# Optimization experiments

Measured on AMD Instinct MI355X. Metric: run time of the kernel, lower is better.

The kernel has to match this reference:

```python
import jax, jax.numpy as jnp
import numpy as np

D_MODEL, D_STATE, EXPAND = 768, 16, 2
D_INNER = D_MODEL * EXPAND
B, L = 2, 2048


def setup_inputs() -> dict:
    key = jax.random.key(0)
    ks = jax.random.split(key, 10)
    s = 0.02  # init scale for projection weights
    return {
        "x": jax.random.normal(ks[0], (B, L, D_MODEL), jnp.float32),
        "in_w": jax.random.normal(ks[1], (D_MODEL, 2 * D_INNER), jnp.float32) * s,
        "conv_w": jax.random.normal(ks[2], (D_INNER, 1, 3), jnp.float32) * 0.1,
        "conv_b": jnp.zeros((D_INNER,), jnp.float32),
        "xproj_w": jax.random.normal(ks[3], (D_INNER, 2 * D_STATE), jnp.float32) * s,
        "dt_w": jax.random.normal(ks[4], (D_INNER, D_INNER), jnp.float32) * s,
        "dt_b": jnp.zeros((D_INNER,), jnp.float32),
        "A_log": jax.random.normal(ks[5], (D_INNER, D_STATE), jnp.float32) * 0.01,
        "D": jnp.ones((D_INNER,), jnp.float32),
        "out_w": jax.random.normal(ks[6], (D_INNER, D_MODEL), jnp.float32) * s,
    }


def reference(x, in_w, conv_w, conv_b, xproj_w, dt_w, dt_b, A_log, D, out_w):
    d_inner = conv_w.shape[0]
    d_state = A_log.shape[1]

    xz = x @ in_w                                   # [B,L,2*d_inner]
    x_c, z = jnp.split(xz, 2, axis=-1)

    # depthwise conv1d, kernel 3, padding 1
    xc = jnp.transpose(x_c, (0, 2, 1))              # [B,d_inner,L]
    xc = jax.lax.conv_general_dilated(
        xc, conv_w, window_strides=(1,), padding=[(1, 1)],
        feature_group_count=d_inner,
        dimension_numbers=("NCH", "OIH", "NCH"))
    xc = xc + conv_b[None, :, None]
    xc = jax.nn.silu(jnp.transpose(xc, (0, 2, 1)))  # [B,L,d_inner]

    Bs, Cs = jnp.split(xc @ xproj_w, 2, axis=-1)    # each [B,L,d_state]
    delta = jax.nn.softplus(xc @ dt_w + dt_b)       # [B,L,d_inner]
    A = -jnp.exp(A_log.astype(jnp.float32))         # [d_inner,d_state]

    deltaA = jnp.exp(jnp.einsum("bld,dn->bldn", delta, A))      # [B,L,d_inner,d_state]
    deltaBx = jnp.einsum("bld,bln->bldn", delta * xc, Bs)        # [B,L,d_inner,d_state]

    def step(h, inp):
        dA_t, dBx_t, c_t = inp                      # [B,d,n],[B,d,n],[B,n]
        h = dA_t * h + dBx_t
        y_t = jnp.einsum("bdn,bn->bd", h, c_t)
        return h, y_t

    h0 = jnp.zeros((x.shape[0], d_inner, d_state), xc.dtype)
    xs = (jnp.moveaxis(deltaA, 1, 0), jnp.moveaxis(deltaBx, 1, 0), jnp.moveaxis(Cs, 1, 0))
    _, ys = jax.lax.scan(step, h0, xs)              # ys: [L,B,d_inner]
    y = jnp.moveaxis(ys, 0, 1) + D * xc             # skip connection

    y = y * jax.nn.silu(z)
    return y @ out_w                                # [B,L,d_model]
```

## Files before the change

### kernel.cpp

```cpp
#include <hip/hip_runtime.h>
#include <cmath>

#define DMODEL 768
#define DINNER 1536
#define NSTATE 16
#define SEQL   2048
#define NCHUNK 32
#define CHLEN  64

#define DT_F32  0
#define DT_BF16 1
#define DT_ZERO 2

typedef __bf16 bf16x8 __attribute__((ext_vector_type(8)));
typedef float  f32x4  __attribute__((ext_vector_type(4)));

typedef __attribute__((address_space(3))) unsigned short lds_us;
typedef const __attribute__((address_space(1))) unsigned short glob_us;

__device__ __forceinline__ void async_cp16(glob_us* g, lds_us* l) {
    __builtin_amdgcn_global_load_lds((const __attribute__((address_space(1))) void*)g,
                                     (__attribute__((address_space(3))) void*)l, 16, 0, 0);
}

__device__ __forceinline__ float bf2f(unsigned short h) {
    union { unsigned u; float f; } v; v.u = ((unsigned)h) << 16; return v.f;
}
__device__ __forceinline__ float bflo(unsigned p) {
    union { unsigned u; float f; } v; v.u = p << 16; return v.f;
}
__device__ __forceinline__ float bfhi(unsigned p) {
    union { unsigned u; float f; } v; v.u = p & 0xFFFF0000u; return v.f;
}
__device__ __forceinline__ unsigned short f2bf(float f) {
    union { float f; unsigned u; } v; v.f = f;
    unsigned r = (v.u + 0x7FFFu + ((v.u >> 16) & 1u)) >> 16;
    return (unsigned short)r;
}
__device__ __forceinline__ float quad_reduce(float y) {
    int yi = __float_as_int(y);
    y += __int_as_float(__builtin_amdgcn_mov_dpp(yi, 0xB1, 0xF, 0xF, true));
    yi = __float_as_int(y);
    y += __int_as_float(__builtin_amdgcn_mov_dpp(yi, 0x4E, 0xF, 0xF, true));
    return y;
}
__device__ int detect_dtype(const void* p) {
    const unsigned* u = (const unsigned*)p;
    int nzlo = 0, band = 0, anynz = 0;
    for (int i = 0; i < 64; ++i) {
        unsigned w = u[i];
        anynz |= (w != 0);
        unsigned lo = w & 0xFFFFu;
        if (lo) {
            ++nzlo;
            unsigned e8 = (lo >> 7) & 0xFF;
            if (e8 >= 0x60 && e8 <= 0x8E) ++band;
        }
    }
    if (nzlo >= 8) return (band * 2 > nzlo) ? DT_BF16 : DT_F32;
    return anynz ? DT_F32 : DT_ZERO;
}
__device__ __forceinline__ float LD(const void* p, size_t i, int dt) {
    if (dt == DT_BF16) return bf2f(((const unsigned short*)p)[i]);
    if (dt == DT_F32)  return ((const float*)p)[i];
    return 0.f;
}

__global__ __launch_bounds__(256) void prep_kernel(
    const void* __restrict__ x, const void* __restrict__ in_w,
    const void* __restrict__ cw, const void* __restrict__ cb,
    const void* __restrict__ xp, const void* __restrict__ dt_w,
    const void* __restrict__ db, const void* __restrict__ Al,
    const void* __restrict__ Dv, const void* __restrict__ out_w,
    unsigned short* __restrict__ xb, unsigned short* __restrict__ inT,
    unsigned short* __restrict__ dtT, unsigned short* __restrict__ outT,
    float* __restrict__ pf)
{
    __shared__ unsigned short tile[64][68];
    __shared__ int dts[6];
    const int blk = blockIdx.x;
    const int t   = threadIdx.x;

    if (blk < 324) {
        if (t == 0) {
            dts[0] = detect_dtype(cw); dts[1] = detect_dtype(cb);
            dts[2] = detect_dtype(db); dts[3] = detect_dtype(Al);
            dts[4] = detect_dtype(Dv); dts[5] = detect_dtype(xp);
        }
        __syncthreads();
        int g = blk * 256 + t;
        if (g >= 82944) return;
        const void* src; int local; int which;
        if      (g <  4608) { src = cw; local = g;         which = 0; }
        else if (g <  6144) { src = cb; local = g - 4608;  which = 1; }
        else if (g <  7680) { src = db; local = g - 6144;  which = 2; }
        else if (g < 32256) { src = Al; local = g - 7680;  which = 3; }
        else if (g < 33792) { src = Dv; local = g - 32256; which = 4; }
        else                { src = xp; local = g - 33792; which = 5; }
        float v = LD(src, local, dts[which]);
        int out = g;
        if (which == 3) v = -__expf(v) * 1.44269504f;
        if (which == 0) out = (local % 3) * DINNER + local / 3;
        pf[out] = v;
    } else if (blk < 1860) {
        if (t == 0) dts[0] = detect_dtype(x);
        __syncthreads();
        const int dt = dts[0];
        size_t i = ((size_t)(blk - 324) * 256 + t) * 8;
        ushort4 o0, o1;
        if (dt == DT_F32) {
            float4 a = *(const float4*)((const float*)x + i);
            float4 b = *(const float4*)((const float*)x + i + 4);
            o0.x = f2bf(a.x); o0.y = f2bf(a.y); o0.z = f2bf(a.z); o0.w = f2bf(a.w);
            o1.x = f2bf(b.x); o1.y = f2bf(b.y); o1.z = f2bf(b.z); o1.w = f2bf(b.w);
        } else if (dt == DT_BF16) {
            o0 = *(const ushort4*)((const unsigned short*)x + i);
            o1 = *(const ushort4*)((const unsigned short*)x + i + 4);
        } else {
            o0 = (ushort4){0,0,0,0}; o1 = (ushort4){0,0,0,0};
        }
        *(ushort4*)&xb[i] = o0;
        *(ushort4*)&xb[i + 4] = o1;
    } else {
        const void* src; unsigned short* dst; int R, C, tx_n, idx;
        if (blk < 2436)      { src = in_w;  dst = inT;  R = 768;  C = 3072; tx_n = 48; idx = blk - 1860; }
        else if (blk < 3012) { src = dt_w;  dst = dtT;  R = 1536; C = 1536; tx_n = 24; idx = blk - 2436; }
        else                 { src = out_w; dst = outT; R = 1536; C = 768;  tx_n = 12; idx = blk - 3012; }
        if (t == 0) dts[0] = detect_dtype(src);
        __syncthreads();
        const int dt = dts[0];
        const int tx = t & 15, ty = t >> 4;
        const int bx = (idx % tx_n) * 64, by = (idx / tx_n) * 64;
        #pragma unroll
        for (int i = 0; i < 4; ++i) {
            int rl = ty + i * 16;
            size_t soff = (size_t)(by + rl) * C + bx + tx * 4;
            ushort4 hv;
            if (dt == DT_F32) {
                float4 v = *(const float4*)((const float*)src + soff);
                hv.x = f2bf(v.x); hv.y = f2bf(v.y); hv.z = f2bf(v.z); hv.w = f2bf(v.w);
            } else if (dt == DT_BF16) {
                hv = *(const ushort4*)((const unsigned short*)src + soff);
            } else {
                hv = (ushort4){0,0,0,0};
            }
            *(ushort4*)&tile[rl][tx * 4] = hv;
        }
        __syncthreads();
        #pragma unroll
        for (int i = 0; i < 4; ++i) {
            int cl = ty + i * 16;
            int m0 = tx * 4;
            ushort4 o;
            o.x = tile[m0 + 0][cl]; o.y = tile[m0 + 1][cl];
            o.z = tile[m0 + 2][cl]; o.w = tile[m0 + 3][cl];
            *(ushort4*)&dst[(size_t)(bx + cl) * R + by + m0] = o;
        }
    }
}

template<int EPI>
__global__ __launch_bounds__(256) void gemm_kernel(
    const unsigned short* __restrict__ A, const unsigned short* __restrict__ Bt,
    void* __restrict__ C0, void* __restrict__ C1, const float* __restrict__ biasf,
    int M, int N, int K)
{
    __shared__ __align__(16) unsigned short As[2][2][128 * 32];
    __shared__ __align__(16) unsigned short Bs[2][2][64 * 32];
    const int t    = threadIdx.x;
    const int m0   = blockIdx.x * 128;
    const int n0   = blockIdx.y * 64;
    const int w    = t >> 6;
    const int lane = t & 63;
    const int wm   = (w >> 1) * 64, wn = (w & 1) * 32;
    const int lm   = lane & 15, quad = lane >> 4;
    const int srow = lane >> 2;
    const int sg   = lane & 3;

    f32x4 acc[4][2] = {};

    auto stage = [&](int k0, int q) {
        #pragma unroll
        for (int ph = 0; ph < 2; ++ph) {
            #pragma unroll
            for (int h = 0; h < 2; ++h) {
                int row = w * 32 + h * 16 + srow;
                int kg  = (sg - (row >> 1)) & 3;
                async_cp16((glob_us*)&A[(size_t)(m0 + row) * K + k0 + ph * 32 + kg * 8],
                           (lds_us*)&As[q][ph][(w * 32 + h * 16) * 32]);
            }
            int brow = w * 16 + srow;
            int bkg  = (sg - (brow >> 1)) & 3;
            async_cp16((glob_us*)&Bt[(size_t)(n0 + brow) * K + k0 + ph * 32 + bkg * 8],
                       (lds_us*)&Bs[q][ph][(w * 16) * 32]);
        }
    };

    stage(0, 0);

    int p = 0;
    for (int k0 = 0; k0 < K; k0 += 64) {
        __syncthreads();
        if (k0 + 64 < K) stage(k0 + 64, p ^ 1);
        #pragma unroll
        for (int ph = 0; ph < 2; ++ph) {
            bf16x8 af[4], bfr[2];
            #pragma unroll
            for (int i = 0; i < 4; ++i) {
                int row = wm + i * 16 + lm;
                int g   = (quad + (row >> 1)) & 3;
                af[i] = *(const bf16x8*)&As[p][ph][row * 32 + g * 8];
            }
            #pragma unroll
            for (int j = 0; j < 2; ++j) {
                int row = wn + j * 16 + lm;
                int g   = (quad + (row >> 1)) & 3;
                bfr[j] = *(const bf16x8*)&Bs[p][ph][row * 32 + g * 8];
            }
            #pragma unroll
            for (int i = 0; i < 4; ++i)
                #pragma unroll
                for (int j = 0; j < 2; ++j)
                    acc[i][j] = __builtin_amdgcn_mfma_f32_16x16x32_bf16(af[i], bfr[j], acc[i][j], 0, 0, 0);
        }
        p ^= 1;
    }

    const int half = N >> 1;
    #pragma unroll
    for (int i = 0; i < 4; ++i) {
        #pragma unroll
        for (int j = 0; j < 2; ++j) {
            int col = n0 + wn + j * 16 + lm;
            #pragma unroll
            for (int r = 0; r < 4; ++r) {
                int row = m0 + wm + i * 16 + quad * 4 + r;
                float v = acc[i][j][r];
                if (EPI == 1) {
                    v += biasf[col];
                    float sp = (v > 20.f) ? v : log1pf(__expf(v));
                    ((unsigned short*)C0)[(size_t)row * N + col] = f2bf(sp);
                } else if (EPI == 2) {
                    ((float*)C0)[(size_t)row * N + col] = v;
                } else {
                    if (col < half) {
                        ((unsigned short*)C0)[(size_t)row * half + col] = f2bf(v);
                    } else {
                        float s = v / (1.f + __expf(-v));
                        ((unsigned short*)C1)[(size_t)row * half + col - half] = f2bf(s);
                    }
                }
            }
        }
    }
}

__global__ __launch_bounds__(256) void conv_silu_kernel(
    const unsigned short* __restrict__ xcpre, const float* __restrict__ cwf,
    const float* __restrict__ cbf, unsigned short* __restrict__ xcb)
{
    const float* cw0 = cwf;
    const float* cw1 = cwf + DINNER;
    const float* cw2 = cwf + 2 * DINNER;
    size_t idx = ((size_t)blockIdx.x * 256 + threadIdx.x) * 8;
    int d8  = (int)(idx % DINNER);
    int row = (int)(idx / DINNER);
    int l   = row % SEQL;
    size_t base = (size_t)row * DINNER + d8;
    uint4 zero = {0, 0, 0, 0};
    uint4 xm = (l > 0)        ? *(const uint4*)&xcpre[base - DINNER] : zero;
    uint4 x0 = *(const uint4*)&xcpre[base];
    uint4 xp = (l < SEQL - 1) ? *(const uint4*)&xcpre[base + DINNER] : zero;
    float4 c0a = *(const float4*)&cw0[d8], c0b = *(const float4*)&cw0[d8 + 4];
    float4 c1a = *(const float4*)&cw1[d8], c1b = *(const float4*)&cw1[d8 + 4];
    float4 c2a = *(const float4*)&cw2[d8], c2b = *(const float4*)&cw2[d8 + 4];
    float4 cba = *(const float4*)&cbf[d8], cbb = *(const float4*)&cbf[d8 + 4];
    const unsigned* mw = (const unsigned*)&xm;
    const unsigned* zw = (const unsigned*)&x0;
    const unsigned* pw = (const unsigned*)&xp;
    const float* C0 = (const float*)&c0a;
    float w0[8] = {c0a.x, c0a.y, c0a.z, c0a.w, c0b.x, c0b.y, c0b.z, c0b.w};
    float w1[8] = {c1a.x, c1a.y, c1a.z, c1a.w, c1b.x, c1b.y, c1b.z, c1b.w};
    float w2[8] = {c2a.x, c2a.y, c2a.z, c2a.w, c2b.x, c2b.y, c2b.z, c2b.w};
    float bb[8] = {cba.x, cba.y, cba.z, cba.w, cbb.x, cbb.y, cbb.z, cbb.w};
    (void)C0;
    unsigned short out[8];
    #pragma unroll
    for (int k = 0; k < 8; ++k) {
        unsigned wm_ = mw[k >> 1], wz = zw[k >> 1], wp = pw[k >> 1];
        float a = (k & 1) ? bfhi(wm_) : bflo(wm_);
        float c = (k & 1) ? bfhi(wz)  : bflo(wz);
        float e = (k & 1) ? bfhi(wp)  : bflo(wp);
        float acc = bb[k] + a * w0[k] + c * w1[k] + e * w2[k];
        float s = acc / (1.f + __expf(-acc));
        out[k] = f2bf(s);
    }
    *(uint4*)&xcb[base] = *(uint4*)out;
}

__global__ __launch_bounds__(128) void xproj_kernel(
    const unsigned short* __restrict__ xcb, const float* __restrict__ wf,
    float* __restrict__ BC)
{
    __shared__ float red[4][32][4];
    const int t = threadIdx.x;
    const int s = t & 31, part = t >> 5;
    const int row0 = blockIdx.x * 4;
    float acc[4] = {0.f, 0.f, 0.f, 0.f};
    for (int k = part * 384; k < (part + 1) * 384; ++k) {
        float wv = wf[k * 32 + s];
        #pragma unroll
        for (int r = 0; r < 4; ++r)
            acc[r] += bf2f(xcb[(size_t)(row0 + r) * DINNER + k]) * wv;
    }
    #pragma unroll
    for (int r = 0; r < 4; ++r) red[part][s][r] = acc[r];
    __syncthreads();
    if (t < 32) {
        #pragma unroll
        for (int r = 0; r < 4; ++r)
            BC[(size_t)(row0 + r) * 32 + t] =
                red[0][t][r] + red[1][t][r] + red[2][t][r] + red[3][t][r];
    }
}

struct GrpA { unsigned dv2[4], xv2[4]; f32x4 Bv[4]; };
struct GrpC { unsigned dv2[4], xv2[4]; f32x4 Bv[4], Cv[4]; };

__device__ __forceinline__ void ldA(GrpA& gp, const unsigned short* pd,
    const unsigned short* px, const float* pbc, int l) {
    #pragma unroll
    for (int j = 0; j < 4; ++j) {
        size_t o = (size_t)(l + j) * DINNER;
        gp.dv2[j] = *(const unsigned*)&pd[o];
        gp.xv2[j] = *(const unsigned*)&px[o];
        gp.Bv[j]  = *(const f32x4*)&pbc[(size_t)(l + j) * 32];
    }
}
__device__ __forceinline__ void ldC(GrpC& gp, const unsigned short* pd,
    const unsigned short* px, const float* pbc, int l) {
    #pragma unroll
    for (int j = 0; j < 4; ++j) {
        size_t o = (size_t)(l + j) * DINNER;
        gp.dv2[j] = *(const unsigned*)&pd[o];
        gp.xv2[j] = *(const unsigned*)&px[o];
        gp.Bv[j]  = *(const f32x4*)&pbc[(size_t)(l + j) * 32];
        gp.Cv[j]  = *(const f32x4*)&pbc[(size_t)(l + j) * 32 + 16];
    }
}
__device__ __forceinline__ void stepA(const GrpA& gp, const f32x4 A2a,
    const f32x4 A2b, f32x4& h0, f32x4& h1, float& sdv0, float& sdv1) {
    #pragma unroll
    for (int j = 0; j < 4; ++j) {
        float dv0 = bflo(gp.dv2[j]), dv1 = bfhi(gp.dv2[j]);
        float xv0 = bflo(gp.xv2[j]), xv1 = bfhi(gp.xv2[j]);
        sdv0 += dv0; sdv1 += dv1;
        f32x4 Bv = gp.Bv[j];
        f32x4 e0, e1;
        e0[0] = __builtin_amdgcn_exp2f(dv0 * A2a[0]);
        e0[1] = __builtin_amdgcn_exp2f(dv0 * A2a[1]);
        e0[2] = __builtin_amdgcn_exp2f(dv0 * A2a[2]);
        e0[3] = __builtin_amdgcn_exp2f(dv0 * A2a[3]);
        e1[0] = __builtin_amdgcn_exp2f(dv1 * A2b[0]);
        e1[1] = __builtin_amdgcn_exp2f(dv1 * A2b[1]);
        e1[2] = __builtin_amdgcn_exp2f(dv1 * A2b[2]);
        e1[3] = __builtin_amdgcn_exp2f(dv1 * A2b[3]);
        h0 = e0 * h0 + (dv0 * xv0) * Bv;
        h1 = e1 * h1 + (dv1 * xv1) * Bv;
    }
}

__global__ __launch_bounds__(256) void scan_phase_a(
    const unsigned short* __restrict__ dlt, const unsigned short* __restrict__ xcb,
    const float* __restrict__ BC, const float* __restrict__ A_log_f,
    unsigned short* __restrict__ P, float* __restrict__ S)
{
    const int t   = threadIdx.x;
    const int q   = t & 3;
    const int dpl = t >> 2;
    const int bid = blockIdx.x;
    const int dg  = bid % 12;
    const int cc  = (bid / 12) % NCHUNK;
    const int b   = bid / (12 * NCHUNK);
    const int d   = (dg * 64 + dpl) * 2;
    f32x4 A2a = *(const f32x4*)&A_log_f[d * 16 + q * 4];
    f32x4 A2b = *(const f32x4*)&A_log_f[(d + 1) * 16 + q * 4];
    f32x4 h0 = (f32x4){0.f, 0.f, 0.f, 0.f};
    f32x4 h1 = (f32x4){0.f, 0.f, 0.f, 0.f};
    float sdv0 = 0.f, sdv1 = 0.f;
    const int row0 = b * SEQL + cc * CHLEN;
    const unsigned short* pd = dlt + (size_t)row0 * DINNER + d;
    const unsigned short* px = xcb + (size_t)row0 * DINNER + d;
    const float* pbc = BC + (size_t)row0 * 32 + q * 4;

    GrpA ga, gb;
    ldA(ga, pd, px, pbc, 0);
    for (int l0 = 0; l0 < CHLEN; l0 += 8) {
        ldA(gb, pd, px, pbc, l0 + 4);
        stepA(ga, A2a, A2b, h0, h1, sdv0, sdv1);
        if (l0 + 8 < CHLEN) ldA(ga, pd, px, pbc, l0 + 8);
        stepA(gb, A2a, A2b, h0, h1, sdv0, sdv1);
    }

    size_t idx = (((size_t)(b * NCHUNK + cc)) * DINNER + d) * 16 + q * 4;
    *(f32x4*)&S[idx] = h0;
    *(f32x4*)&S[idx + 16] = h1;
    ushort4 p0, p1;
    p0.x = f2bf(__builtin_amdgcn_exp2f(sdv0 * A2a[0]));
    p0.y = f2bf(__builtin_amdgcn_exp2f(sdv0 * A2a[1]));
    p0.z = f2bf(__builtin_amdgcn_exp2f(sdv0 * A2a[2]));
    p0.w = f2bf(__builtin_amdgcn_exp2f(sdv0 * A2a[3]));
    p1.x = f2bf(__builtin_amdgcn_exp2f(sdv1 * A2b[0]));
    p1.y = f2bf(__builtin_amdgcn_exp2f(sdv1 * A2b[1]));
    p1.z = f2bf(__builtin_amdgcn_exp2f(sdv1 * A2b[2]));
    p1.w = f2bf(__builtin_amdgcn_exp2f(sdv1 * A2b[3]));
    *(ushort4*)&P[idx] = p0;
    *(ushort4*)&P[idx + 16] = p1;
}

__global__ __launch_bounds__(256) void scan_combine(
    const unsigned short* __restrict__ P, float* __restrict__ S)
{
    int t = blockIdx.x * 256 + threadIdx.x;
    int b = t / (DINNER * NSTATE);
    int dn = t % (DINNER * NSTATE);
    const size_t stride = (size_t)(DINNER * NSTATE);
    size_t idx = (size_t)b * NCHUNK * stride + dn;
    float Pv = bf2f(P[idx]);
    float Sv = S[idx];
    float H = 0.f;
    for (int c = 0; c < NCHUNK; ++c) {
        float Pn = 0.f, Sn = 0.f;
        if (c + 1 < NCHUNK) {
            Pn = bf2f(P[idx + stride]);
            Sn = S[idx + stride];
        }
        S[idx] = H;
        H = Pv * H + Sv;
        Pv = Pn; Sv = Sn;
        idx += stride;
    }
}

__global__ __launch_bounds__(256) void scan_phase_c(
    const unsigned short* __restrict__ dlt, const unsigned short* __restrict__ xcb,
    const float* __restrict__ BC, const unsigned short* __restrict__ zg,
    const float* __restrict__ A_log_f, const float* __restrict__ D_f,
    const float* __restrict__ Hin, unsigned short* __restrict__ yg)
{
    const int t   = threadIdx.x;
    const int q   = t & 3;
    const int dpl = t >> 2;
    const int bid = blockIdx.x;
    const int dg  = bid % 12;
    const int cc  = (bid / 12) % NCHUNK;
    const int b   = bid / (12 * NCHUNK);
    const int d   = (dg * 64 + dpl) * 2;
    f32x4 A2a = *(const f32x4*)&A_log_f[d * 16 + q * 4];
    f32x4 A2b = *(const f32x4*)&A_log_f[(d + 1) * 16 + q * 4];
    size_t hidx = (((size_t)(b * NCHUNK + cc)) * DINNER + d) * 16 + q * 4;
    f32x4 h0 = *(const f32x4*)&Hin[hidx];
    f32x4 h1 = *(const f32x4*)&Hin[hidx + 16];
    const float Dd0 = D_f[d], Dd1 = D_f[d + 1];
    const int row0 = b * SEQL + cc * CHLEN;
    const unsigned short* pd = dlt + (size_t)row0 * DINNER + d;
    const unsigned short* px = xcb + (size_t)row0 * DINNER + d;
    const unsigned short* pz = zg  + (size_t)row0 * DINNER + d;
    unsigned short* py = yg + (size_t)row0 * DINNER + d;
    const float* pbc = BC + (size_t)row0 * 32 + q * 4;

    GrpC ga, gb;
    auto stepC = [&](const GrpC& gp, int l) {
        #pragma unroll
        for (int j = 0; j < 4; ++j) {
            float dv0 = bflo(gp.dv2[j]), dv1 = bfhi(gp.dv2[j]);
            float xv0 = bflo(gp.xv2[j]), xv1 = bfhi(gp.xv2[j]);
            f32x4 Bv = gp.Bv[j], Cv = gp.Cv[j];
            f32x4 e0, e1;
            e0[0] = __builtin_amdgcn_exp2f(dv0 * A2a[0]);
            e0[1] = __builtin_amdgcn_exp2f(dv0 * A2a[1]);
            e0[2] = __builtin_amdgcn_exp2f(dv0 * A2a[2]);
            e0[3] = __builtin_amdgcn_exp2f(dv0 * A2a[3]);
            e1[0] = __builtin_amdgcn_exp2f(dv1 * A2b[0]);
            e1[1] = __builtin_amdgcn_exp2f(dv1 * A2b[1]);
            e1[2] = __builtin_amdgcn_exp2f(dv1 * A2b[2]);
            e1[3] = __builtin_amdgcn_exp2f(dv1 * A2b[3]);
            h0 = e0 * h0 + (dv0 * xv0) * Bv;
            h1 = e1 * h1 + (dv1 * xv1) * Bv;
            f32x4 y0v = h0 * Cv;
            f32x4 y1v = h1 * Cv;
            float y0 = quad_reduce(y0v[0] + y0v[1] + y0v[2] + y0v[3]);
            float y1 = quad_reduce(y1v[0] + y1v[1] + y1v[2] + y1v[3]);
            if (j == q) {
                unsigned zp = *(const unsigned*)&pz[(size_t)(l + j) * DINNER];
                ushort2 o;
                o.x = f2bf((y0 + Dd0 * xv0) * bflo(zp));
                o.y = f2bf((y1 + Dd1 * xv1) * bfhi(zp));
                *(ushort2*)&py[(size_t)(l + j) * DINNER] = o;
            }
        }
    };

    ldC(ga, pd, px, pbc, 0);
    for (int l0 = 0; l0 < CHLEN; l0 += 8) {
        ldC(gb, pd, px, pbc, l0 + 4);
        stepC(ga, l0);
        if (l0 + 8 < CHLEN) ldC(ga, pd, px, pbc, l0 + 8);
        stepC(gb, l0 + 4);
    }
}

__global__ void guard_kernel(float* out, int code)
{
    if (threadIdx.x == 0 && blockIdx.x == 0 && code) out[0] = (float)code;
}

extern "C" void kernel_launch(void* const* d_in, const int* in_sizes, int n_in,
                              void* d_out, int out_size, void* d_ws, size_t ws_size,
                              hipStream_t stream) {
    static const int EXPECTED[10] = {3145728, 2359296, 4608, 1536, 49152,
                                     2359296, 1536, 24576, 1536, 1179648};
    bool ok = (n_in == 10);
    if (ok) for (int i = 0; i < 10; ++i) ok = ok && (in_sizes[i] == EXPECTED[i]);
    int code = 0;
    if (!ok) code = 2000;
    else if (ws_size < 67895296ULL) code = 3000;
    if (code) { guard_kernel<<<1, 64, 0, stream>>>((float*)d_out, code); return; }

    const void* x       = d_in[0];
    const void* in_w    = d_in[1];
    const void* conv_w  = d_in[2];
    const void* conv_b  = d_in[3];
    const void* xproj_w = d_in[4];
    const void* dt_w    = d_in[5];
    const void* dt_b    = d_in[6];
    const void* A_log   = d_in[7];
    const void* Dvec    = d_in[8];
    const void* out_w   = d_in[9];

    char* ws = (char*)d_ws;
    float* conv_w_f = (float*)(ws + 0);
    float* conv_b_f = (float*)(ws + 18432);
    float* dt_b_f   = (float*)(ws + 24576);
    float* A_log_f  = (float*)(ws + 30720);
    float* D_f      = (float*)(ws + 129024);
    float* xproj_f  = (float*)(ws + 135168);
    unsigned short* xb    = (unsigned short*)(ws + 524288);
    unsigned short* inT   = (unsigned short*)(ws + 6815744);
    unsigned short* yg    = (unsigned short*)(ws + 524288);
    unsigned short* dtT   = (unsigned short*)(ws + 13107200);
    unsigned short* outT  = (unsigned short*)(ws + 17825792);
    unsigned short* xcpre = (unsigned short*)(ws + 20185088);
    unsigned short* dlt   = xcpre;
    float*          BC    = (float*)(ws + 32768000);
    unsigned short* zg    = (unsigned short*)(ws + 33292288);
    unsigned short* xcb   = (unsigned short*)(ws + 45875200);
    float*          scanS = (float*)(ws + 58458112);
    unsigned short* scanP = (unsigned short*)(ws + 64749568);

    prep_kernel<<<3300, 256, 0, stream>>>(x, in_w, conv_w, conv_b, xproj_w, dt_w,
                                          dt_b, A_log, Dvec, out_w,
                                          xb, inT, dtT, outT, (float*)ws);

    gemm_kernel<3><<<dim3(32, 48), 256, 0, stream>>>(xb, inT, (void*)xcpre, (void*)zg,
                                                     nullptr, 4096, 3072, 768);
    conv_silu_kernel<<<(4096 * DINNER / 8) / 256, 256, 0, stream>>>(xcpre, conv_w_f, conv_b_f, xcb);
    xproj_kernel<<<1024, 128, 0, stream>>>(xcb, xproj_f, BC);
    gemm_kernel<1><<<dim3(32, 24), 256, 0, stream>>>(xcb, dtT, (void*)dlt, nullptr,
                                                     dt_b_f, 4096, 1536, 1536);
    scan_phase_a<<<768, 256, 0, stream>>>(dlt, xcb, BC, A_log_f, scanP, scanS);
    scan_combine<<<192, 256, 0, stream>>>(scanP, scanS);
    scan_phase_c<<<768, 256, 0, stream>>>(dlt, xcb, BC, zg, A_log_f, D_f, scanS, yg);
    gemm_kernel<2><<<dim3(32, 12), 256, 0, stream>>>(yg, outT, d_out, nullptr,
                                                    nullptr, 4096, 768, 1536);
}
```

Measured before the change: 316.6 us.

## Fuse x_proj into dt GEMM and widen scan kernels to four channels per thread

Removes the separate scalar xproj kernel. The x_proj weights are transposed to bf16 in prep and appended as extra N columns (one more 64-wide tile) to the dt_proj GEMM, whose new epilogue writes softplus delta for the first 1536 columns and fp32 B/C for the next 32. The scan phase A and C kernels now handle four channels per thread instead of two, with wider loads and half as many blocks. The trade-offs are lower parallelism in the scan, higher register pressure, and B/C computed from bf16 weights instead of fp32.

```diff
diff --git a/kernel.cpp b/kernel.cpp
--- a/kernel.cpp
+++ b/kernel.cpp
@@ -74,7 +74,7 @@
     const void* __restrict__ Dv, const void* __restrict__ out_w,
     unsigned short* __restrict__ xb, unsigned short* __restrict__ inT,
     unsigned short* __restrict__ dtT, unsigned short* __restrict__ outT,
-    float* __restrict__ pf)
+    unsigned short* __restrict__ xpT, float* __restrict__ pf)
 {
     __shared__ unsigned short tile[64][68];
     __shared__ int dts[6];
@@ -121,7 +121,7 @@
         }
         *(ushort4*)&xb[i] = o0;
         *(ushort4*)&xb[i + 4] = o1;
-    } else {
+    } else if (blk < 3300) {
         const void* src; unsigned short* dst; int R, C, tx_n, idx;
         if (blk < 2436)      { src = in_w;  dst = inT;  R = 768;  C = 3072; tx_n = 48; idx = blk - 1860; }
         else if (blk < 3012) { src = dt_w;  dst = dtT;  R = 1536; C = 1536; tx_n = 24; idx = blk - 2436; }
@@ -156,12 +156,23 @@
             o.z = tile[m0 + 2][cl]; o.w = tile[m0 + 3][cl];
             *(ushort4*)&dst[(size_t)(bx + cl) * R + by + m0] = o;
         }
+    } else {
+        if (t == 0) dts[0] = detect_dtype(xp);
+        __syncthreads();
+        const int dt = dts[0];
+        int r = (blk - 3300) * 256 + t;
+        #pragma unroll 4
+        for (int c = 0; c < 32; ++c) {
+            float v = LD(xp, (size_t)r * 32 + c, dt);
+            xpT[(size_t)c * DINNER + r] = f2bf(v);
+        }
     }
 }
 
 template<int EPI>
 __global__ __launch_bounds__(256) void gemm_kernel(
     const unsigned short* __restrict__ A, const unsigned short* __restrict__ Bt,
+    const unsigned short* __restrict__ Bt2,
     void* __restrict__ C0, void* __restrict__ C1, const float* __restrict__ biasf,
     int M, int N, int K)
 {
@@ -191,7 +202,15 @@
             }
             int brow = w * 16 + srow;
             int bkg  = (sg - (brow >> 1)) & 3;
-            async_cp16((glob_us*)&Bt[(size_t)(n0 + brow) * K + k0 + ph * 32 + bkg * 8],
+            const unsigned short* bsrc;
+            if (EPI == 4) {
+                int gr = n0 + brow;
+                bsrc = (gr < 1536) ? &Bt[(size_t)gr * K]
+                                   : &Bt2[(size_t)(((gr < 1567) ? gr : 1567) - 1536) * K];
+            } else {
+                bsrc = &Bt[(size_t)(n0 + brow) * K];
+            }
+            async_cp16((glob_us*)&bsrc[k0 + ph * 32 + bkg * 8],
                        (lds_us*)&Bs[q][ph][(w * 16) * 32]);
         }
     };
@@ -236,18 +255,22 @@
             for (int r = 0; r < 4; ++r) {
                 int row = m0 + wm + i * 16 + quad * 4 + r;
                 float v = acc[i][j][r];
-                if (EPI == 1) {
-                    v += biasf[col];
-                    float sp = (v > 20.f) ? v : log1pf(__expf(v));
-                    ((unsigned short*)C0)[(size_t)row * N + col] = f2bf(sp);
-                } else if (EPI == 2) {
+                if (EPI == 2) {
                     ((float*)C0)[(size_t)row * N + col] = v;
-                } else {
+                } else if (EPI == 3) {
                     if (col < half) {
                         ((unsigned short*)C0)[(size_t)row * half + col] = f2bf(v);
                     } else {
                         float s = v / (1.f + __expf(-v));
                         ((unsigned short*)C1)[(size_t)row * half + col - half] = f2bf(s);
+                    }
+                } else {
+                    if (col < 1536) {
+                        v += biasf[col];
+                        float sp = (v > 20.f) ? v : log1pf(__expf(v));
+                        ((unsigned short*)C0)[(size_t)row * 1536 + col] = f2bf(sp);
+                    } else if (col < 1568) {
+                        ((float*)C1)[(size_t)row * 32 + (col - 1536)] = v;
                     }
                 }
             }
@@ -278,12 +301,10 @@
     const unsigned* mw = (const unsigned*)&xm;
     const unsigned* zw = (const unsigned*)&x0;
     const unsigned* pw = (const unsigned*)&xp;
-    const float* C0 = (const float*)&c0a;
     float w0[8] = {c0a.x, c0a.y, c0a.z, c0a.w, c0b.x, c0b.y, c0b.z, c0b.w};
     float w1[8] = {c1a.x, c1a.y, c1a.z, c1a.w, c1b.x, c1b.y, c1b.z, c1b.w};
     float w2[8] = {c2a.x, c2a.y, c2a.z, c2a.w, c2b.x, c2b.y, c2b.z, c2b.w};
     float bb[8] = {cba.x, cba.y, cba.z, cba.w, cbb.x, cbb.y, cbb.z, cbb.w};
-    (void)C0;
     unsigned short out[8];
     #pragma unroll
     for (int k = 0; k < 8; ++k) {
@@ -298,75 +319,28 @@
     *(uint4*)&xcb[base] = *(uint4*)out;
 }
 
-__global__ __launch_bounds__(128) void xproj_kernel(
-    const unsigned short* __restrict__ xcb, const float* __restrict__ wf,
-    float* __restrict__ BC)
-{
-    __shared__ float red[4][32][4];
-    const int t = threadIdx.x;
-    const int s = t & 31, part = t >> 5;
-    const int row0 = blockIdx.x * 4;
-    float acc[4] = {0.f, 0.f, 0.f, 0.f};
-    for (int k = part * 384; k < (part + 1) * 384; ++k) {
-        float wv = wf[k * 32 + s];
-        #pragma unroll
-        for (int r = 0; r < 4; ++r)
-            acc[r] += bf2f(xcb[(size_t)(row0 + r) * DINNER + k]) * wv;
-    }
-    #pragma unroll
-    for (int r = 0; r < 4; ++r) red[part][s][r] = acc[r];
-    __syncthreads();
-    if (t < 32) {
-        #pragma unroll
-        for (int r = 0; r < 4; ++r)
-            BC[(size_t)(row0 + r) * 32 + t] =
-                red[0][t][r] + red[1][t][r] + red[2][t][r] + red[3][t][r];
-    }
-}
-
-struct GrpA { unsigned dv2[4], xv2[4]; f32x4 Bv[4]; };
-struct GrpC { unsigned dv2[4], xv2[4]; f32x4 Bv[4], Cv[4]; };
-
-__device__ __forceinline__ void ldA(GrpA& gp, const unsigned short* pd,
+struct Grp4A { uint2 dv[4], xv[4]; f32x4 Bv[4]; };
+struct Grp4C { uint2 dv[4], xv[4]; f32x4 Bv[4], Cv[4]; };
+
+__device__ __forceinline__ void ldA4(Grp4A& gp, const unsigned short* pd,
     const unsigned short* px, const float* pbc, int l) {
     #pragma unroll
     for (int j = 0; j < 4; ++j) {
         size_t o = (size_t)(l + j) * DINNER;
-        gp.dv2[j] = *(const unsigned*)&pd[o];
-        gp.xv2[j] = *(const unsigned*)&px[o];
-        gp.Bv[j]  = *(const f32x4*)&pbc[(size_t)(l + j) * 32];
-    }
-}
-__device__ __forceinline__ void ldC(GrpC& gp, const unsigned short* pd,
+        gp.dv[j] = *(const uint2*)&pd[o];
+        gp.xv[j] = *(const uint2*)&px[o];
+        gp.Bv[j] = *(const f32x4*)&pbc[(size_t)(l + j) * 32];
+    }
+}
+__device__ __forceinline__ void ldC4(Grp4C& gp, const unsigned short* pd,
     const unsigned short* px, const float* pbc, int l) {
     #pragma unroll
     for (int j = 0; j < 4; ++j) {
         size_t o = (size_t)(l + j) * DINNER;
-        gp.dv2[j] = *(const unsigned*)&pd[o];
-        gp.xv2[j] = *(const unsigned*)&px[o];
-        gp.Bv[j]  = *(const f32x4*)&pbc[(size_t)(l + j) * 32];
-        gp.Cv[j]  = *(const f32x4*)&pbc[(size_t)(l + j) * 32 + 16];
-    }
-}
-__device__ __forceinline__ void stepA(const GrpA& gp, const f32x4 A2a,
-    const f32x4 A2b, f32x4& h0, f32x4& h1, float& sdv0, float& sdv1) {
-    #pragma unroll
-    for (int j = 0; j < 4; ++j) {
-        float dv0 = bflo(gp.dv2[j]), dv1 = bfhi(gp.dv2[j]);
-        float xv0 = bflo(gp.xv2[j]), xv1 = bfhi(gp.xv2[j]);
-        sdv0 += dv0; sdv1 += dv1;
-        f32x4 Bv = gp.Bv[j];
-        f32x4 e0, e1;
-        e0[0] = __builtin_amdgcn_exp2f(dv0 * A2a[0]);
-        e0[1] = __builtin_amdgcn_exp2f(dv0 * A2a[1]);
-        e0[2] = __builtin_amdgcn_exp2f(dv0 * A2a[2]);
-        e0[3] = __builtin_amdgcn_exp2f(dv0 * A2a[3]);
-        e1[0] = __builtin_amdgcn_exp2f(dv1 * A2b[0]);
-        e1[1] = __builtin_amdgcn_exp2f(dv1 * A2b[1]);
-        e1[2] = __builtin_amdgcn_exp2f(dv1 * A2b[2]);
-        e1[3] = __builtin_amdgcn_exp2f(dv1 * A2b[3]);
-        h0 = e0 * h0 + (dv0 * xv0) * Bv;
-        h1 = e1 * h1 + (dv1 * xv1) * Bv;
+        gp.dv[j] = *(const uint2*)&pd[o];
+        gp.xv[j] = *(const uint2*)&px[o];
+        gp.Bv[j] = *(const f32x4*)&pbc[(size_t)(l + j) * 32];
+        gp.Cv[j] = *(const f32x4*)&pbc[(size_t)(l + j) * 32 + 16];
     }
 }
 
@@ -379,43 +353,60 @@
     const int q   = t & 3;
     const int dpl = t >> 2;
     const int bid = blockIdx.x;
-    const int dg  = bid % 12;
-    const int cc  = (bid / 12) % NCHUNK;
-    const int b   = bid / (12 * NCHUNK);
-    const int d   = (dg * 64 + dpl) * 2;
-    f32x4 A2a = *(const f32x4*)&A_log_f[d * 16 + q * 4];
-    f32x4 A2b = *(const f32x4*)&A_log_f[(d + 1) * 16 + q * 4];
-    f32x4 h0 = (f32x4){0.f, 0.f, 0.f, 0.f};
-    f32x4 h1 = (f32x4){0.f, 0.f, 0.f, 0.f};
-    float sdv0 = 0.f, sdv1 = 0.f;
+    const int dg  = bid % 6;
+    const int cc  = (bid / 6) % NCHUNK;
+    const int b   = bid / (6 * NCHUNK);
+    const int d   = (dg * 64 + dpl) * 4;
+    f32x4 A2[4];
+    #pragma unroll
+    for (int dd = 0; dd < 4; ++dd)
+        A2[dd] = *(const f32x4*)&A_log_f[(d + dd) * 16 + q * 4];
+    f32x4 h[4] = {};
+    float sdv[4] = {0.f, 0.f, 0.f, 0.f};
     const int row0 = b * SEQL + cc * CHLEN;
     const unsigned short* pd = dlt + (size_t)row0 * DINNER + d;
     const unsigned short* px = xcb + (size_t)row0 * DINNER + d;
     const float* pbc = BC + (size_t)row0 * 32 + q * 4;
 
-    GrpA ga, gb;
-    ldA(ga, pd, px, pbc, 0);
+    auto stepA = [&](const Grp4A& gp) {
+        #pragma unroll
+        for (int j = 0; j < 4; ++j) {
+            float dvv[4] = {bflo(gp.dv[j].x), bfhi(gp.dv[j].x), bflo(gp.dv[j].y), bfhi(gp.dv[j].y)};
+            float xvv[4] = {bflo(gp.xv[j].x), bfhi(gp.xv[j].x), bflo(gp.xv[j].y), bfhi(gp.xv[j].y)};
+            f32x4 Bv = gp.Bv[j];
+            #pragma unroll
+            for (int dd = 0; dd < 4; ++dd) {
+                sdv[dd] += dvv[dd];
+                f32x4 e;
+                e[0] = __builtin_amdgcn_exp2f(dvv[dd] * A2[dd][0]);
+                e[1] = __builtin_amdgcn_exp2f(dvv[dd] * A2[dd][1]);
+                e[2] = __builtin_amdgcn_exp2f(dvv[dd] * A2[dd][2]);
+                e[3] = __builtin_amdgcn_exp2f(dvv[dd] * A2[dd][3]);
+                h[dd] = e * h[dd] + (dvv[dd] * xvv[dd]) * Bv;
+            }
+        }
+    };
+
+    Grp4A ga, gb;
+    ldA4(ga, pd, px, pbc, 0);
     for (int l0 = 0; l0 < CHLEN; l0 += 8) {
-        ldA(gb, pd, px, pbc, l0 + 4);
-        stepA(ga, A2a, A2b, h0, h1, sdv0, sdv1);
-        if (l0 + 8 < CHLEN) ldA(ga, pd, px, pbc, l0 + 8);
-        stepA(gb, A2a, A2b, h0, h1, sdv0, sdv1);
+        ldA4(gb, pd, px, pbc, l0 + 4);
+        stepA(ga);
+        if (l0 + 8 < CHLEN) ldA4(ga, pd, px, pbc, l0 + 8);
+        stepA(gb);
     }
 
     size_t idx = (((size_t)(b * NCHUNK + cc)) * DINNER + d) * 16 + q * 4;
-    *(f32x4*)&S[idx] = h0;
-    *(f32x4*)&S[idx + 16] = h1;
-    ushort4 p0, p1;
-    p0.x = f2bf(__builtin_amdgcn_exp2f(sdv0 * A2a[0]));
-    p0.y = f2bf(__builtin_amdgcn_exp2f(sdv0 * A2a[1]));
-    p0.z = f2bf(__builtin_amdgcn_exp2f(sdv0 * A2a[2]));
-    p0.w = f2bf(__builtin_amdgcn_exp2f(sdv0 * A2a[3]));
-    p1.x = f2bf(__builtin_amdgcn_exp2f(sdv1 * A2b[0]));
-    p1.y = f2bf(__builtin_amdgcn_exp2f(sdv1 * A2b[1]));
-    p1.z = f2bf(__builtin_amdgcn_exp2f(sdv1 * A2b[2]));
-    p1.w = f2bf(__builtin_amdgcn_exp2f(sdv1 * A2b[3]));
-    *(ushort4*)&P[idx] = p0;
-    *(ushort4*)&P[idx + 16] = p1;
+    #pragma unroll
+    for (int dd = 0; dd < 4; ++dd) {
+        *(f32x4*)&S[idx + dd * 16] = h[dd];
+        ushort4 pq;
+        pq.x = f2bf(__builtin_amdgcn_exp2f(sdv[dd] * A2[dd][0]));
+        pq.y = f2bf(__builtin_amdgcn_exp2f(sdv[dd] * A2[dd][1]));
+        pq.z = f2bf(__builtin_amdgcn_exp2f(sdv[dd] * A2[dd][2]));
+        pq.w = f2bf(__builtin_amdgcn_exp2f(sdv[dd] * A2[dd][3]));
+        *(ushort4*)&P[idx + dd * 16] = pq;
+    }
 }
 
 __global__ __launch_bounds__(256) void scan_combine(
@@ -452,16 +443,21 @@
     const int q   = t & 3;
     const int dpl = t >> 2;
     const int bid = blockIdx.x;
-    const int dg  = bid % 12;
-    const int cc  = (bid / 12) % NCHUNK;
-    const int b   = bid / (12 * NCHUNK);
-    const int d   = (dg * 64 + dpl) * 2;
-    f32x4 A2a = *(const f32x4*)&A_log_f[d * 16 + q * 4];
-    f32x4 A2b = *(const f32x4*)&A_log_f[(d + 1) * 16 + q * 4];
+    const int dg  = bid % 6;
+    const int cc  = (bid / 6) % NCHUNK;
+    const int b   = bid / (6 * NCHUNK);
+    const int d   = (dg * 64 + dpl) * 4;
+    f32x4 A2[4];
+    float Dd[4];
+    #pragma unroll
+    for (int dd = 0; dd < 4; ++dd) {
+        A2[dd] = *(const f32x4*)&A_log_f[(d + dd) * 16 + q * 4];
+        Dd[dd] = D_f[d + dd];
+    }
     size_t hidx = (((size_t)(b * NCHUNK + cc)) * DINNER + d) * 16 + q * 4;
-    f32x4 h0 = *(const f32x4*)&Hin[hidx];
-    f32x4 h1 = *(const f32x4*)&Hin[hidx + 16];
-    const float Dd0 = D_f[d], Dd1 = D_f[d + 1];
+    f32x4 h[4];
+    #pragma unroll
+    for (int dd = 0; dd < 4; ++dd) h[dd] = *(const f32x4*)&Hin[hidx + dd * 16];
     const int row0 = b * SEQL + cc * CHLEN;
     const unsigned short* pd = dlt + (size_t)row0 * DINNER + d;
     const unsigned short* px = xcb + (size_t)row0 * DINNER + d;
@@ -469,43 +465,43 @@
     unsigned short* py = yg + (size_t)row0 * DINNER + d;
     const float* pbc = BC + (size_t)row0 * 32 + q * 4;
 
-    GrpC ga, gb;
-    auto stepC = [&](const GrpC& gp, int l) {
+    auto stepC = [&](const Grp4C& gp, int l) {
         #pragma unroll
         for (int j = 0; j < 4; ++j) {
-            float dv0 = bflo(gp.dv2[j]), dv1 = bfhi(gp.dv2[j]);
-            float xv0 = bflo(gp.xv2[j]), xv1 = bfhi(gp.xv2[j]);
+            float dvv[4] = {bflo(gp.dv[j].x), bfhi(gp.dv[j].x), bflo(gp.dv[j].y), bfhi(gp.dv[j].y)};
+            float xvv[4] = {bflo(gp.xv[j].x), bfhi(gp.xv[j].x), bflo(gp.xv[j].y), bfhi(gp.xv[j].y)};
             f32x4 Bv = gp.Bv[j], Cv = gp.Cv[j];
-            f32x4 e0, e1;
-            e0[0] = __builtin_amdgcn_exp2f(dv0 * A2a[0]);
-            e0[1] = __builtin_amdgcn_exp2f(dv0 * A2a[1]);
-            e0[2] = __builtin_amdgcn_exp2f(dv0 * A2a[2]);
-            e0[3] = __builtin_amdgcn_exp2f(dv0 * A2a[3]);
-            e1[0] = __builtin_amdgcn_exp2f(dv1 * A2b[0]);
-            e1[1] = __builtin_amdgcn_exp2f(dv1 * A2b[1]);
-            e1[2] = __builtin_amdgcn_exp2f(dv1 * A2b[2]);
-            e1[3] = __builtin_amdgcn_exp2f(dv1 * A2b[3]);
-            h0 = e0 * h0 + (dv0 * xv0) * Bv;
-            h1 = e1 * h1 + (dv1 * xv1) * Bv;
-            f32x4 y0v = h0 * Cv;
-            f32x4 y1v = h1 * Cv;
-            float y0 = quad_reduce(y0v[0] + y0v[1] + y0v[2] + y0v[3]);
-            float y1 = quad_reduce(y1v[0] + y1v[1] + y1v[2] + y1v[3]);
+            float y[4];
+            #pragma unroll
+            for (int dd = 0; dd < 4; ++dd) {
+                f32x4 e;
+                e[0] = __builtin_amdgcn_exp2f(dvv[dd] * A2[dd][0]);
+                e[1] = __builtin_amdgcn_exp2f(dvv[dd] * A2[dd][1]);
+                e[2] = __builtin_amdgcn_exp2f(dvv[dd] * A2[dd][2]);
+                e[3] = __builtin_amdgcn_exp2f(dvv[dd] * A2[dd][3]);
+                h[dd] = e * h[dd] + (dvv[dd] * xvv[dd]) * Bv;
+                f32x4 yv = h[dd] * Cv;
+                y[dd] = quad_reduce(yv[0] + yv[1] + yv[2] + yv[3]);
+            }
             if (j == q) {
-                unsigned zp = *(const unsigned*)&pz[(size_t)(l + j) * DINNER];
-                ushort2 o;
-                o.x = f2bf((y0 + Dd0 * xv0) * bflo(zp));
-                o.y = f2bf((y1 + Dd1 * xv1) * bfhi(zp));
-                *(ushort2*)&py[(size_t)(l + j) * DINNER] = o;
+                uint2 zp = *(const uint2*)&pz[(size_t)(l + j) * DINNER];
+                float zv[4] = {bflo(zp.x), bfhi(zp.x), bflo(zp.y), bfhi(zp.y)};
+                ushort4 o;
+                o.x = f2bf((y[0] + Dd[0] * xvv[0]) * zv[0]);
+                o.y = f2bf((y[1] + Dd[1] * xvv[1]) * zv[1]);
+                o.z = f2bf((y[2] + Dd[2] * xvv[2]) * zv[2]);
+                o.w = f2bf((y[3] + Dd[3] * xvv[3]) * zv[3]);
+                *(ushort4*)&py[(size_t)(l + j) * DINNER] = o;
             }
         }
     };
 
-    ldC(ga, pd, px, pbc, 0);
+    Grp4C ga, gb;
+    ldC4(ga, pd, px, pbc, 0);
     for (int l0 = 0; l0 < CHLEN; l0 += 8) {
-        ldC(gb, pd, px, pbc, l0 + 4);
+        ldC4(gb, pd, px, pbc, l0 + 4);
         stepC(ga, l0);
-        if (l0 + 8 < CHLEN) ldC(ga, pd, px, pbc, l0 + 8);
+        if (l0 + 8 < CHLEN) ldC4(ga, pd, px, pbc, l0 + 8);
         stepC(gb, l0 + 4);
     }
 }
@@ -544,7 +540,7 @@
     float* dt_b_f   = (float*)(ws + 24576);
     float* A_log_f  = (float*)(ws + 30720);
     float* D_f      = (float*)(ws + 129024);
-    float* xproj_f  = (float*)(ws + 135168);
+    unsigned short* xpT   = (unsigned short*)(ws + 331776);
     unsigned short* xb    = (unsigned short*)(ws + 524288);
     unsigned short* inT   = (unsigned short*)(ws + 6815744);
     unsigned short* yg    = (unsigned short*)(ws + 524288);
@@ -558,19 +554,18 @@
     float*          scanS = (float*)(ws + 58458112);
     unsigned short* scanP = (unsigned short*)(ws + 64749568);
 
-    prep_kernel<<<3300, 256, 0, stream>>>(x, in_w, conv_w, conv_b, xproj_w, dt_w,
+    prep_kernel<<<3306, 256, 0, stream>>>(x, in_w, conv_w, conv_b, xproj_w, dt_w,
                                           dt_b, A_log, Dvec, out_w,
-                                          xb, inT, dtT, outT, (float*)ws);
-
-    gemm_kernel<3><<<dim3(32, 48), 256, 0, stream>>>(xb, inT, (void*)xcpre, (void*)zg,
-                                                     nullptr, 4096, 3072, 768);
+                                          xb, inT, dtT, outT, xpT, (float*)ws);
+
+    gemm_kernel<3><<<dim3(32, 48), 256, 0, stream>>>(xb, inT, nullptr, (void*)xcpre,
+                                                     (void*)zg, nullptr, 4096, 3072, 768);
     conv_silu_kernel<<<(4096 * DINNER / 8) / 256, 256, 0, stream>>>(xcpre, conv_w_f, conv_b_f, xcb);
-    xproj_kernel<<<1024, 128, 0, stream>>>(xcb, xproj_f, BC);
-    gemm_kernel<1><<<dim3(32, 24), 256, 0, stream>>>(xcb, dtT, (void*)dlt, nullptr,
-                                                     dt_b_f, 4096, 1536, 1536);
-    scan_phase_a<<<768, 256, 0, stream>>>(dlt, xcb, BC, A_log_f, scanP, scanS);
+    gemm_kernel<4><<<dim3(32, 25), 256, 0, stream>>>(xcb, dtT, xpT, (void*)dlt,
+                                                     (void*)BC, dt_b_f, 4096, 1536, 1536);
+    scan_phase_a<<<384, 256, 0, stream>>>(dlt, xcb, BC, A_log_f, scanP, scanS);
     scan_combine<<<192, 256, 0, stream>>>(scanP, scanS);
-    scan_phase_c<<<768, 256, 0, stream>>>(dlt, xcb, BC, zg, A_log_f, D_f, scanS, yg);
-    gemm_kernel<2><<<dim3(32, 12), 256, 0, stream>>>(yg, outT, d_out, nullptr,
-                                                    nullptr, 4096, 768, 1536);
-}
+    scan_phase_c<<<384, 256, 0, stream>>>(dlt, xcb, BC, zg, A_log_f, D_f, scanS, yg);
+    gemm_kernel<2><<<dim3(32, 12), 256, 0, stream>>>(yg, outT, nullptr, d_out,
+                                                     nullptr, nullptr, 4096, 768, 1536);
+}
```

After: 320.2 us. Within noise of the previous version (+1.2%).

## Fuse x-projection into dt GEMM as extra output columns

Applied to the files above, without the earlier changes.

Removes the separate scalar xproj kernel and computes B/C projections inside the dt-projection MFMA GEMM. A bf16 transposed copy of xproj_w is added in prep, and the grid gets one extra 64-column tile whose rows 1536-1567 come from that copy. The epilogue applies bias+softplus to the dt columns and writes raw fp32 for the B/C columns. This saves one launch and a slow scalar reduction over xcb, but B/C now use bf16 weights, and the fused GEMM uses a simpler single-buffer-pair layout than gemm_kernel.

```diff
diff --git a/kernel.cpp b/kernel.cpp
--- a/kernel.cpp
+++ b/kernel.cpp
@@ -74,7 +74,7 @@
     const void* __restrict__ Dv, const void* __restrict__ out_w,
     unsigned short* __restrict__ xb, unsigned short* __restrict__ inT,
     unsigned short* __restrict__ dtT, unsigned short* __restrict__ outT,
-    float* __restrict__ pf)
+    unsigned short* __restrict__ xpT, float* __restrict__ pf)
 {
     __shared__ unsigned short tile[64][68];
     __shared__ int dts[6];
@@ -121,7 +121,7 @@
         }
         *(ushort4*)&xb[i] = o0;
         *(ushort4*)&xb[i + 4] = o1;
-    } else {
+    } else if (blk < 3300) {
         const void* src; unsigned short* dst; int R, C, tx_n, idx;
         if (blk < 2436)      { src = in_w;  dst = inT;  R = 768;  C = 3072; tx_n = 48; idx = blk - 1860; }
         else if (blk < 3012) { src = dt_w;  dst = dtT;  R = 1536; C = 1536; tx_n = 24; idx = blk - 2436; }
@@ -155,6 +155,16 @@
             o.x = tile[m0 + 0][cl]; o.y = tile[m0 + 1][cl];
             o.z = tile[m0 + 2][cl]; o.w = tile[m0 + 3][cl];
             *(ushort4*)&dst[(size_t)(bx + cl) * R + by + m0] = o;
+        }
+    } else {
+        if (t == 0) dts[0] = detect_dtype(xp);
+        __syncthreads();
+        const int dt = dts[0];
+        int r = (blk - 3300) * 256 + t;
+        #pragma unroll 4
+        for (int c = 0; c < 32; ++c) {
+            float v = LD(xp, (size_t)r * 32 + c, dt);
+            xpT[(size_t)c * DINNER + r] = f2bf(v);
         }
     }
 }
@@ -236,11 +246,7 @@
             for (int r = 0; r < 4; ++r) {
                 int row = m0 + wm + i * 16 + quad * 4 + r;
                 float v = acc[i][j][r];
-                if (EPI == 1) {
-                    v += biasf[col];
-                    float sp = (v > 20.f) ? v : log1pf(__expf(v));
-                    ((unsigned short*)C0)[(size_t)row * N + col] = f2bf(sp);
-                } else if (EPI == 2) {
+                if (EPI == 2) {
                     ((float*)C0)[(size_t)row * N + col] = v;
                 } else {
                     if (col < half) {
@@ -249,6 +255,93 @@
                         float s = v / (1.f + __expf(-v));
                         ((unsigned short*)C1)[(size_t)row * half + col - half] = f2bf(s);
                     }
+                }
+            }
+        }
+    }
+}
+
+__global__ __launch_bounds__(256) void gemm_fused_kernel(
+    const unsigned short* __restrict__ A, const unsigned short* __restrict__ Bt,
+    const unsigned short* __restrict__ Bt2,
+    unsigned short* __restrict__ C0, float* __restrict__ C1,
+    const float* __restrict__ biasf, int M, int K)
+{
+    __shared__ __align__(16) unsigned short As[2][128 * 32];
+    __shared__ __align__(16) unsigned short Bs[2][64 * 32];
+    const int t    = threadIdx.x;
+    const int m0   = blockIdx.x * 128;
+    const int n0   = blockIdx.y * 64;
+    const int w    = t >> 6;
+    const int lane = t & 63;
+    const int wm   = (w >> 1) * 64, wn = (w & 1) * 32;
+    const int lm   = lane & 15, quad = lane >> 4;
+    const int srow = lane >> 2;
+    const int sg   = lane & 3;
+
+    const int arow0 = w * 32 + srow;
+    const int arow1 = w * 32 + 16 + srow;
+    const int akg0  = (sg - (arow0 >> 1)) & 3;
+    const int akg1  = (sg - (arow1 >> 1)) & 3;
+    const int brow  = w * 16 + srow;
+    const int bkg   = (sg - (brow >> 1)) & 3;
+    const int gr    = n0 + brow;
+    const unsigned short* aB0 = &A[(size_t)(m0 + arow0) * K + akg0 * 8];
+    const unsigned short* aB1 = &A[(size_t)(m0 + arow1) * K + akg1 * 8];
+    const unsigned short* bB  = (gr < 1536)
+        ? &Bt[(size_t)gr * K + bkg * 8]
+        : &Bt2[(size_t)(((gr < 1567) ? gr : 1567) - 1536) * K + bkg * 8];
+
+    f32x4 acc[4][2] = {};
+
+    auto stage = [&](int k0, int q) {
+        async_cp16((glob_us*)(aB0 + k0), (lds_us*)&As[q][(w * 32) * 32]);
+        async_cp16((glob_us*)(aB1 + k0), (lds_us*)&As[q][(w * 32 + 16) * 32]);
+        async_cp16((glob_us*)(bB  + k0), (lds_us*)&Bs[q][(w * 16) * 32]);
+    };
+
+    stage(0, 0);
+
+    int p = 0;
+    for (int k0 = 0; k0 < K; k0 += 32) {
+        __syncthreads();
+        if (k0 + 32 < K) stage(k0 + 32, p ^ 1);
+        bf16x8 af[4], bfr[2];
+        #pragma unroll
+        for (int i = 0; i < 4; ++i) {
+            int row = wm + i * 16 + lm;
+            int g   = (quad + (row >> 1)) & 3;
+            af[i] = *(const bf16x8*)&As[p][row * 32 + g * 8];
+        }
+        #pragma unroll
+        for (int j = 0; j < 2; ++j) {
+            int row = wn + j * 16 + lm;
+            int g   = (quad + (row >> 1)) & 3;
+            bfr[j] = *(const bf16x8*)&Bs[p][row * 32 + g * 8];
+        }
+        #pragma unroll
+        for (int i = 0; i < 4; ++i)
+            #pragma unroll
+            for (int j = 0; j < 2; ++j)
+                acc[i][j] = __builtin_amdgcn_mfma_f32_16x16x32_bf16(af[i], bfr[j], acc[i][j], 0, 0, 0);
+        p ^= 1;
+    }
+
+    #pragma unroll
+    for (int i = 0; i < 4; ++i) {
+        #pragma unroll
+        for (int j = 0; j < 2; ++j) {
+            int col = n0 + wn + j * 16 + lm;
+            #pragma unroll
+            for (int r = 0; r < 4; ++r) {
+                int row = m0 + wm + i * 16 + quad * 4 + r;
+                float v = acc[i][j][r];
+                if (col < 1536) {
+                    v += biasf[col];
+                    float sp = (v > 20.f) ? v : log1pf(__expf(v));
+                    C0[(size_t)row * 1536 + col] = f2bf(sp);
+                } else if (col < 1568) {
+                    C1[(size_t)row * 32 + (col - 1536)] = v;
                 }
             }
         }
@@ -278,12 +371,10 @@
     const unsigned* mw = (const unsigned*)&xm;
     const unsigned* zw = (const unsigned*)&x0;
     const unsigned* pw = (const unsigned*)&xp;
-    const float* C0 = (const float*)&c0a;
     float w0[8] = {c0a.x, c0a.y, c0a.z, c0a.w, c0b.x, c0b.y, c0b.z, c0b.w};
     float w1[8] = {c1a.x, c1a.y, c1a.z, c1a.w, c1b.x, c1b.y, c1b.z, c1b.w};
     float w2[8] = {c2a.x, c2a.y, c2a.z, c2a.w, c2b.x, c2b.y, c2b.z, c2b.w};
     float bb[8] = {cba.x, cba.y, cba.z, cba.w, cbb.x, cbb.y, cbb.z, cbb.w};
-    (void)C0;
     unsigned short out[8];
     #pragma unroll
     for (int k = 0; k < 8; ++k) {
@@ -296,32 +387,6 @@
         out[k] = f2bf(s);
     }
     *(uint4*)&xcb[base] = *(uint4*)out;
-}
-
-__global__ __launch_bounds__(128) void xproj_kernel(
-    const unsigned short* __restrict__ xcb, const float* __restrict__ wf,
-    float* __restrict__ BC)
-{
-    __shared__ float red[4][32][4];
-    const int t = threadIdx.x;
-    const int s = t & 31, part = t >> 5;
-    const int row0 = blockIdx.x * 4;
-    float acc[4] = {0.f, 0.f, 0.f, 0.f};
-    for (int k = part * 384; k < (part + 1) * 384; ++k) {
-        float wv = wf[k * 32 + s];
-        #pragma unroll
-        for (int r = 0; r < 4; ++r)
-            acc[r] += bf2f(xcb[(size_t)(row0 + r) * DINNER + k]) * wv;
-    }
-    #pragma unroll
-    for (int r = 0; r < 4; ++r) red[part][s][r] = acc[r];
-    __syncthreads();
-    if (t < 32) {
-        #pragma unroll
-        for (int r = 0; r < 4; ++r)
-            BC[(size_t)(row0 + r) * 32 + t] =
-                red[0][t][r] + red[1][t][r] + red[2][t][r] + red[3][t][r];
-    }
 }
 
 struct GrpA { unsigned dv2[4], xv2[4]; f32x4 Bv[4]; };
@@ -544,7 +609,7 @@
     float* dt_b_f   = (float*)(ws + 24576);
     float* A_log_f  = (float*)(ws + 30720);
     float* D_f      = (float*)(ws + 129024);
-    float* xproj_f  = (float*)(ws + 135168);
+    unsigned short* xpT   = (unsigned short*)(ws + 331776);
     unsigned short* xb    = (unsigned short*)(ws + 524288);
     unsigned short* inT   = (unsigned short*)(ws + 6815744);
     unsigned short* yg    = (unsigned short*)(ws + 524288);
@@ -558,19 +623,18 @@
     float*          scanS = (float*)(ws + 58458112);
     unsigned short* scanP = (unsigned short*)(ws + 64749568);
 
-    prep_kernel<<<3300, 256, 0, stream>>>(x, in_w, conv_w, conv_b, xproj_w, dt_w,
+    prep_kernel<<<3306, 256, 0, stream>>>(x, in_w, conv_w, conv_b, xproj_w, dt_w,
                                           dt_b, A_log, Dvec, out_w,
-                                          xb, inT, dtT, outT, (float*)ws);
-
-    gemm_kernel<3><<<dim3(32, 48), 256, 0, stream>>>(xb, inT, (void*)xcpre, (void*)zg,
-                                                     nullptr, 4096, 3072, 768);
+                                          xb, inT, dtT, outT, xpT, (float*)ws);
+
+    gemm_kernel<3><<<dim3(32, 48), 256, 0, stream>>>(xb, inT, (void*)xcpre,
+                                                     (void*)zg, nullptr, 4096, 3072, 768);
     conv_silu_kernel<<<(4096 * DINNER / 8) / 256, 256, 0, stream>>>(xcpre, conv_w_f, conv_b_f, xcb);
-    xproj_kernel<<<1024, 128, 0, stream>>>(xcb, xproj_f, BC);
-    gemm_kernel<1><<<dim3(32, 24), 256, 0, stream>>>(xcb, dtT, (void*)dlt, nullptr,
-                                                     dt_b_f, 4096, 1536, 1536);
+    gemm_fused_kernel<<<dim3(32, 25), 256, 0, stream>>>(xcb, dtT, xpT, dlt, BC,
+                                                        dt_b_f, 4096, 1536);
     scan_phase_a<<<768, 256, 0, stream>>>(dlt, xcb, BC, A_log_f, scanP, scanS);
     scan_combine<<<192, 256, 0, stream>>>(scanP, scanS);
     scan_phase_c<<<768, 256, 0, stream>>>(dlt, xcb, BC, zg, A_log_f, D_f, scanS, yg);
-    gemm_kernel<2><<<dim3(32, 12), 256, 0, stream>>>(yg, outT, d_out, nullptr,
-                                                    nullptr, 4096, 768, 1536);
-}
+    gemm_kernel<2><<<dim3(32, 12), 256, 0, stream>>>(yg, outT, d_out,
+                                                     nullptr, nullptr, 4096, 768, 1536);
+}
```

Measured after the change: 299.7 us. -5.3%, faster.
